# Optimization experiments

Measured on AMD Instinct MI355X. Metric: run time of the kernel, lower is better.

Reference implementation:

```python
import jax, jax.numpy as jnp
import numpy as np

B, L, M = 4, 16384, 256
HID, FDIM, INNER, ODIM = 512, 128, 128, 3
HEADS, DH = 2, 64
NFREQ = 16  # feature_dim // (2 * input_dim)
ALPHA = 10.0
SIGMA_Q = 128.0
SIGMA_LS = (128.0, 32.0, 8.0)


def setup_inputs() -> dict:
    key = jax.random.key(0)
    ks = jax.random.split(key, 16)
    s = 0.02
    nl = len(SIGMA_LS)
    return {
        "x": jax.random.uniform(ks[0], (B, L, 4), jnp.float32),
        "tokens": jax.random.normal(ks[1], (B, M, HID), jnp.float32),
        "w_query": jax.random.normal(ks[2], (FDIM, HID), jnp.float32) * s,
        "b_query": jnp.zeros((HID,), jnp.float32),
        "w_to_q": jax.random.normal(ks[3], (HID, INNER), jnp.float32) * s,
        "w_to_kv": jax.random.normal(ks[4], (HID, 2 * INNER), jnp.float32) * s,
        "w_to_out": jax.random.normal(ks[5], (INNER, HID), jnp.float32) * s,
        "b_to_out": jnp.zeros((HID,), jnp.float32),
        "w_band": jax.random.normal(ks[6], (nl, FDIM, HID), jnp.float32) * s,
        "b_band": jnp.zeros((nl, HID), jnp.float32),
        "w_mod": jax.random.normal(ks[7], (nl, HID, HID), jnp.float32) * s,
        "b_mod": jnp.zeros((nl, HID), jnp.float32),
        "w_hv": jax.random.normal(ks[8], (nl - 1, HID, HID), jnp.float32) * s,
        "b_hv": jnp.zeros((nl - 1, HID), jnp.float32),
        "w_out": jax.random.normal(ks[9], (nl, HID, ODIM), jnp.float32) * s,
        "b_out": jnp.zeros((nl, ODIM), jnp.float32),
        "Dd": 8, "Hh": 16, "Ww": 16, "Tt": 8,
    }


def _calc_gamma(grid, omegas):
    # grid: [L, 4]; omegas: [NFREQ] -> gamma: [L, 4*2*NFREQ] = [L, FDIM]
    arg = jnp.pi * grid[:, :, None] * omegas[None, None, :]
    return jnp.concatenate([jnp.sin(arg), jnp.cos(arg)], axis=-1).reshape(grid.shape[0], -1)


def reference(x, tokens, w_query, b_query, w_to_q, w_to_kv, w_to_out, b_to_out,
              w_band, b_band, w_mod, b_mod, w_hv, b_hv, w_out, b_out, Dd, Hh, Ww, Tt):
    Bn, Ln, _ = x.shape
    m = tokens.shape[1]
    grid = x[0]  # grid shared across batch, exactly as in the torch module (uses x[0])

    # relative-position bias (ALiBi-like) from approximate patch indices
    z_i = (grid[:, 0] * Dd).astype(jnp.int32)
    y_i = (grid[:, 1] * Hh).astype(jnp.int32)
    x_i = (grid[:, 2] * Ww).astype(jnp.int32)
    t_i = (grid[:, 3] * Tt).astype(jnp.int32)
    idx = ((t_i * Dd + z_i) * Hh + y_i) * Ww + x_i  # [L]
    n_tot = Dd * Hh * Ww * Tt
    t = idx.astype(jnp.float32) / n_tot
    tok_pos = (jnp.arange(m, dtype=jnp.float32) + 0.5) / m
    bias = -ALPHA * (t[:, None] - tok_pos[None, :]) ** 2  # [L, m]

    # Fourier-feature query path (shared across batch)
    omegas_q = jnp.logspace(1.0, np.log10(SIGMA_Q), NFREQ, dtype=jnp.float32)
    x_q = jax.nn.relu(_calc_gamma(grid, omegas_q) @ w_query + b_query)  # [L, HID]

    # cross attention with additive bias
    q = (x_q @ w_to_q).reshape(Ln, HEADS, DH).transpose(1, 0, 2)  # [H, L, Dh]
    kv = tokens @ w_to_kv  # [B, m, 2*INNER]
    k, v = jnp.split(kv, 2, axis=-1)
    k = k.reshape(Bn, m, HEADS, DH).transpose(0, 2, 1, 3)  # [B, H, m, Dh]
    v = v.reshape(Bn, m, HEADS, DH).transpose(0, 2, 1, 3)
    sim = jnp.einsum('hld,bhmd->bhlm', q, k) * (DH ** -0.5) + bias[None, None]
    attn = jax.nn.softmax(sim, axis=-1)
    out = jnp.einsum('bhlm,bhmd->bhld', attn, v)
    out = out.transpose(0, 2, 1, 3).reshape(Bn, Ln, HEADS * DH)
    modv = out @ w_to_out + b_to_out  # [B, L, HID]

    # modulated MLP chain with residual hv accumulation
    total = jnp.zeros((Bn, Ln, w_out.shape[-1]), dtype=x.dtype)
    hv = None
    for kk in range(len(SIGMA_LS)):
        omg = jnp.logspace(1.0, np.log10(SIGMA_LS[kk]), NFREQ, dtype=jnp.float32)
        h_l = jax.nn.relu(_calc_gamma(grid, omg) @ w_band[kk] + b_band[kk])  # [L, HID]
        m_l = jax.nn.relu(h_l[None] + modv @ w_mod[kk] + b_mod[kk])  # [B, L, HID]
        if kk == 0:
            hv = m_l
        else:
            hv = jax.nn.relu((m_l + hv) @ w_hv[kk - 1] + b_hv[kk - 1])
        total = total + hv @ w_out[kk] + b_out[kk]
    return total  # [B, L, ODIM]
```

## Files before the change

### kernel.cpp

```cpp
#include <hip/hip_runtime.h>

#define L_N   16384
#define B_N   4
#define M_N   256
#define HID_N 512
#define PI_F  3.14159265358979323846f

typedef short short8 __attribute__((ext_vector_type(8)));
typedef float f32x4 __attribute__((ext_vector_type(4)));

__device__ __forceinline__ ushort f2bf(float f) {
  uint u = __float_as_uint(f);
  uint r = u + 0x7FFF + ((u >> 16) & 1);
  return (ushort)(r >> 16);
}
__device__ __forceinline__ float bf2f(ushort s) {
  return __uint_as_float(((uint)s) << 16);
}
__device__ __forceinline__ void gld_lds16(const void* g, void* s) {
  __builtin_amdgcn_global_load_lds((const __attribute__((address_space(1))) void*)g,
                                   (__attribute__((address_space(3))) void*)s, 16, 0, 0);
}

__global__ __launch_bounds__(256) void k_wt_all(
    const float* __restrict__ w_query, const float* __restrict__ w_to_q,
    const float* __restrict__ w_to_kv, const float* __restrict__ w_to_out,
    const float* __restrict__ w_band, const float* __restrict__ w_mod,
    const float* __restrict__ w_hv,
    ushort* __restrict__ wq_t, ushort* __restrict__ wtq_t,
    ushort* __restrict__ wkv_t, ushort* __restrict__ wto_t,
    ushort* __restrict__ wb_t, ushort* __restrict__ wm_t, ushort* __restrict__ whv_t) {
  __shared__ float t[32][33];
  int tb = blockIdx.x;
  const float* in; ushort* out; int R, C;
  if (tb < 64)        { in = w_query;  out = wq_t;  R = 128; C = 512; }
  else if (tb < 128)  { tb -= 64;  in = w_to_q;   out = wtq_t; R = 512; C = 128; }
  else if (tb < 256)  { tb -= 128; in = w_to_kv;  out = wkv_t; R = 512; C = 256; }
  else if (tb < 320)  { tb -= 256; in = w_to_out; out = wto_t; R = 128; C = 512; }
  else if (tb < 512)  { tb -= 320; int kk = tb >> 6; tb &= 63;
                        in = w_band + (size_t)kk * 65536; out = wb_t + (size_t)kk * 65536; R = 128; C = 512; }
  else if (tb < 1280) { tb -= 512; int kk = tb >> 8; tb &= 255;
                        in = w_mod + (size_t)kk * 262144; out = wm_t + (size_t)kk * 262144; R = 512; C = 512; }
  else                { tb -= 1280; int kk = tb >> 8; tb &= 255;
                        in = w_hv + (size_t)kk * 262144; out = whv_t + (size_t)kk * 262144; R = 512; C = 512; }
  int nbx = C >> 5;
  int bx = (tb % nbx) * 32, by = (tb / nbx) * 32;
  int tx = threadIdx.x & 31, ty = threadIdx.x >> 5;
#pragma unroll
  for (int j = 0; j < 32; j += 8) t[ty + j][tx] = in[(size_t)(by + ty + j) * C + bx + tx];
  __syncthreads();
#pragma unroll
  for (int j = 0; j < 32; j += 8)
    out[(size_t)(bx + ty + j) * R + by + tx] = f2bf(t[tx][ty + j]);
}

__global__ __launch_bounds__(256) void k_cvt(const float* __restrict__ in,
                                             ushort* __restrict__ out, int n4) {
  int i = blockIdx.x * 256 + threadIdx.x;
  if (i >= n4) return;
  float4 v = *(const float4*)&in[(size_t)i * 4];
  ushort* o = &out[(size_t)i * 4];
  o[0] = f2bf(v.x); o[1] = f2bf(v.y); o[2] = f2bf(v.z); o[3] = f2bf(v.w);
}

__global__ __launch_bounds__(256) void k_gamma(const float* __restrict__ x,
                                               ushort* __restrict__ gout) {
  __shared__ float om[16];
  const float lgs[4] = {2.1072099696478683f, 2.1072099696478683f,
                        1.5051499783199058f, 0.9030899869919435f};
  int spec = blockIdx.y;
  float lg = lgs[spec];
  int tid = threadIdx.x;
  if (tid < 16) om[tid] = powf(10.0f, 1.0f + (float)tid * ((lg - 1.0f) * (1.0f / 15.0f)));
  __syncthreads();
  int l0 = blockIdx.x * 16;
  int idx0 = tid * 8;
  int row = idx0 >> 7, f0 = idx0 & 127;
  int c = f0 >> 5;
  float g = x[(size_t)(l0 + row) * 4 + c];
  float base = PI_F * g;
  int w0 = f0 & 31;
  bool is_cos = (w0 >= 16);
  short8 o;
#pragma unroll
  for (int j = 0; j < 8; ++j) {
    int jf = (w0 + j) & 15;
    float arg = base * om[jf];
    float v = is_cos ? __cosf(arg) : __sinf(arg);
    o[j] = (short)f2bf(v);
  }
  *(short8*)&gout[(size_t)spec * L_N * 128 + (size_t)(l0 + row) * 128 + f0] = o;
}

__global__ __launch_bounds__(256) void k_tpos(const float* __restrict__ x,
                                              const int* dD, const int* dH,
                                              const int* dW, const int* dT,
                                              float* __restrict__ tbuf) {
  int l = blockIdx.x * 256 + threadIdx.x;
  float g0 = x[(size_t)l * 4 + 0], g1 = x[(size_t)l * 4 + 1];
  float g2 = x[(size_t)l * 4 + 2], g3 = x[(size_t)l * 4 + 3];
  int Dd = dD[0], Hh = dH[0], Ww = dW[0], Tt = dT[0];
  int zi = (int)(g0 * (float)Dd), yi = (int)(g1 * (float)Hh);
  int xi = (int)(g2 * (float)Ww), ti = (int)(g3 * (float)Tt);
  int idx = ((ti * Dd + zi) * Hh + yi) * Ww + xi;
  tbuf[l] = (float)idx / (float)(Dd * Hh * Ww * Tt);
}

__global__ __launch_bounds__(256, 4) void k_gemm2(
    const ushort* __restrict__ A, long long sA,
    const ushort* __restrict__ Wt, long long sWt,
    const float* __restrict__ bias, int sBias,
    const ushort* __restrict__ add1,
    const ushort* add2, long long sAdd2,
    ushort* C, long long sC,
    const float* __restrict__ wout,
    float* __restrict__ opb,
    int zoff,
    int N, int K, int do_relu,
    int nbx, int nby, int nz) {
  __shared__ __align__(16) ushort S[128 * 64 * 2];
  __shared__ float woutL[384];
  ushort* As = S;
  ushort* Ws = S + 128 * 64;
  int tid = threadIdx.x;
  int lane = tid & 63, wid = tid >> 6;

  int nwg = nbx * nby * nz;
  int gid0 = blockIdx.x;
  int q = nwg >> 3, r = nwg & 7;
  int xcd = gid0 & 7, rank = gid0 >> 3;
  int sid = (xcd < r) ? (xcd * (q + 1) + rank) : (r * (q + 1) + (xcd - r) * q + rank);
  int z = sid / (nbx * nby);
  int rem = sid - z * (nbx * nby);
  int n0 = (rem % nbx) * 128, r0 = (rem / nbx) * 128;

  A += (size_t)z * sA;
  C += (size_t)z * sC;
  const ushort* Wtp = Wt + (size_t)z * sWt;
  const float* biasp = bias ? bias + (size_t)z * sBias : nullptr;
  const ushort* a2p = add2 ? add2 + (size_t)z * sAdd2 : nullptr;
  int wr = wid >> 1, wc = wid & 1;
  int ksm = K >> 6;

  f32x4 acc[4][4];
#pragma unroll
  for (int i = 0; i < 4; ++i)
#pragma unroll
    for (int j = 0; j < 4; ++j) acc[i][j] = (f32x4)0.0f;

  for (int t = 0; t < ksm; ++t) {
#pragma unroll
    for (int j = 0; j < 4; ++j) {
      int sig = j * 256 + wid * 64 + lane;
      int rr = sig >> 3, ph = sig & 7, sl = ph ^ (rr & 7);
      gld_lds16(&A[(size_t)(r0 + rr) * K + t * 64 + sl * 8], &As[(size_t)(j * 256 + wid * 64) * 8]);
      gld_lds16(&Wtp[(size_t)(n0 + rr) * K + t * 64 + sl * 8], &Ws[(size_t)(j * 256 + wid * 64) * 8]);
    }
    __syncthreads();
#pragma unroll
    for (int ks = 0; ks < 2; ++ks) {
      short8 af[4], bg[4];
#pragma unroll
      for (int fm = 0; fm < 4; ++fm) {
        int row = wr * 64 + fm * 16 + (lane & 15);
        af[fm] = *(const short8*)&As[row * 64 + (((ks * 4 + (lane >> 4)) ^ (row & 7)) * 8)];
      }
#pragma unroll
      for (int fn = 0; fn < 4; ++fn) {
        int nl = wc * 64 + fn * 16 + (lane & 15);
        bg[fn] = *(const short8*)&Ws[nl * 64 + (((ks * 4 + (lane >> 4)) ^ (nl & 7)) * 8)];
      }
#pragma unroll
      for (int fm = 0; fm < 4; ++fm)
#pragma unroll
        for (int fn = 0; fn < 4; ++fn)
          acc[fm][fn] = __builtin_amdgcn_mfma_f32_16x16x32_bf16(af[fm], bg[fn], acc[fm][fn], 0, 0, 0);
    }
    __syncthreads();
  }

  if (wout && tid < 128) {
    woutL[tid * 3 + 0] = wout[(size_t)(n0 + tid) * 3 + 0];
    woutL[tid * 3 + 1] = wout[(size_t)(n0 + tid) * 3 + 1];
    woutL[tid * 3 + 2] = wout[(size_t)(n0 + tid) * 3 + 2];
  }

  float* Ls = (float*)S;
  int row = tid >> 3;
  int c0 = (tid & 7) * 16;
#pragma unroll
  for (int fm = 0; fm < 4; ++fm) {
    if (fm) __syncthreads();
#pragma unroll
    for (int fn = 0; fn < 4; ++fn)
#pragma unroll
      for (int reg = 0; reg < 4; ++reg) {
        int lr = wr * 16 + (lane >> 4) * 4 + reg;
        int lc = wc * 64 + fn * 16 + (lane & 15);
        Ls[lr * 132 + lc] = acc[fm][fn][reg];
      }
    __syncthreads();
    int gr = r0 + (row >> 4) * 64 + fm * 16 + (row & 15);
    float so0 = 0.0f, so1 = 0.0f, so2 = 0.0f;
#pragma unroll
    for (int hh = 0; hh < 2; ++hh) {
      int cc = c0 + hh * 8;
      float v[8];
#pragma unroll
      for (int j = 0; j < 8; ++j) v[j] = Ls[row * 132 + cc + j];
      if (biasp) {
#pragma unroll
        for (int j = 0; j < 8; ++j) v[j] += biasp[n0 + cc + j];
      }
      if (add1) {
        short8 a1 = *(const short8*)&add1[(size_t)gr * N + n0 + cc];
#pragma unroll
        for (int j = 0; j < 8; ++j) v[j] += bf2f((ushort)a1[j]);
      }
      if (do_relu) {
#pragma unroll
        for (int j = 0; j < 8; ++j) v[j] = fmaxf(v[j], 0.0f);
      }
      if (a2p) {
        short8 a2 = *(const short8*)&a2p[(size_t)gr * N + n0 + cc];
#pragma unroll
        for (int j = 0; j < 8; ++j) v[j] += bf2f((ushort)a2[j]);
      }
      if (wout) {
#pragma unroll
        for (int j = 0; j < 8; ++j) {
          so0 = fmaf(v[j], woutL[(cc + j) * 3 + 0], so0);
          so1 = fmaf(v[j], woutL[(cc + j) * 3 + 1], so1);
          so2 = fmaf(v[j], woutL[(cc + j) * 3 + 2], so2);
        }
      }
      short8 ov;
#pragma unroll
      for (int j = 0; j < 8; ++j) ov[j] = (short)f2bf(v[j]);
      *(short8*)&C[(size_t)gr * N + n0 + cc] = ov;
    }
    if (wout) {
      so0 += __shfl_down(so0, 4); so1 += __shfl_down(so1, 4); so2 += __shfl_down(so2, 4);
      so0 += __shfl_down(so0, 2); so1 += __shfl_down(so1, 2); so2 += __shfl_down(so2, 2);
      so0 += __shfl_down(so0, 1); so1 += __shfl_down(so1, 1); so2 += __shfl_down(so2, 1);
      if ((tid & 7) == 0) {
        int bx = n0 >> 7;
        size_t oi = (((size_t)bx * 4 + (zoff + z)) * L_N + gr) * 3;
        opb[oi + 0] = so0; opb[oi + 1] = so1; opb[oi + 2] = so2;
      }
    }
  }
}

__global__ __launch_bounds__(256) void k_outred(const float* __restrict__ opb,
                                                const float* __restrict__ b_out,
                                                float* __restrict__ out) {
  int i = blockIdx.x * 256 + threadIdx.x;
  if (i >= B_N * L_N) return;
  float a0 = b_out[0] + b_out[3] + b_out[6];
  float a1 = b_out[1] + b_out[4] + b_out[7];
  float a2 = b_out[2] + b_out[5] + b_out[8];
  const size_t SS = (size_t)4 * B_N * L_N * 3;
#pragma unroll
  for (int slot = 0; slot < 3; ++slot)
#pragma unroll
    for (int bx = 0; bx < 4; ++bx) {
      const float* p = opb + slot * SS + (((size_t)bx * B_N * L_N) + i) * 3;
      a0 += p[0]; a1 += p[1]; a2 += p[2];
    }
  out[(size_t)i * 3 + 0] = a0;
  out[(size_t)i * 3 + 1] = a1;
  out[(size_t)i * 3 + 2] = a2;
}

__global__ __launch_bounds__(256) void k_rearr(const ushort* __restrict__ kvtmp,
                                               ushort* __restrict__ kbuf,
                                               ushort* __restrict__ vtb) {
  int i = blockIdx.x * 256 + threadIdx.x;
  int col = i & 255, row = i >> 8;
  int b = row >> 8, m = row & 255;
  ushort v = kvtmp[i];
  if (col < 128)
    kbuf[((size_t)b * 256 + m) * 128 + col] = v;
  else
    vtb[(size_t)b * 128 * 256 + (size_t)(col - 128) * 256 + m] = v;
}

__global__ __launch_bounds__(256) void k_attn_m(const ushort* __restrict__ qbuf,
                                                const float* __restrict__ tbuf,
                                                const ushort* __restrict__ kbuf,
                                                const ushort* __restrict__ vtb,
                                                ushort* __restrict__ attn) {
  __shared__ __align__(16) ushort Kt[256 * 64];
  __shared__ __align__(16) ushort Vt[64 * 256];
  __shared__ __align__(16) ushort Qs[64 * 64];
  __shared__ __align__(16) ushort Pw[4][16 * 40];
  __shared__ float ts[64];
  int tid = threadIdx.x;
  int lane = tid & 63, wid = tid >> 6;
  int l0 = blockIdx.x * 64;
  int h = blockIdx.y;
  int z = blockIdx.z;
  const ushort* kbuf_b = kbuf + (size_t)z * M_N * 128;
  const ushort* vtb_b = vtb + (size_t)z * 128 * M_N;
  ushort* attn_b = attn + (size_t)z * L_N * 128;
#pragma unroll
  for (int j = 0; j < 8; ++j) {
    int sig = j * 256 + wid * 64 + lane;
    int m = sig >> 3, ph = sig & 7, sl = ph ^ (m & 7);
    gld_lds16(&kbuf_b[(size_t)m * 128 + h * 64 + sl * 8], &Kt[(size_t)(j * 256 + wid * 64) * 8]);
  }
#pragma unroll
  for (int j = 0; j < 8; ++j) {
    int sig = j * 256 + wid * 64 + lane;
    int d = sig >> 5, ph = sig & 31, sl = ph ^ ((d & 7) << 2);
    gld_lds16(&vtb_b[(size_t)(h * 64 + d) * 256 + sl * 8], &Vt[(size_t)(j * 256 + wid * 64) * 8]);
  }
#pragma unroll
  for (int j = 0; j < 2; ++j) {
    int sig = j * 256 + wid * 64 + lane;
    int q = sig >> 3, ph = sig & 7, sl = ph ^ (q & 7);
    gld_lds16(&qbuf[(size_t)(l0 + q) * 128 + h * 64 + sl * 8], &Qs[(size_t)(j * 256 + wid * 64) * 8]);
  }
  if (tid < 64) ts[tid] = tbuf[l0 + tid];
  __syncthreads();

  f32x4 s_acc[16];
#pragma unroll
  for (int fn = 0; fn < 16; ++fn) s_acc[fn] = (f32x4)0.0f;
#pragma unroll
  for (int ks = 0; ks < 2; ++ks) {
    int qrow = wid * 16 + (lane & 15);
    short8 aq = *(const short8*)&Qs[qrow * 64 + (((ks * 4 + (lane >> 4)) ^ (qrow & 7)) * 8)];
#pragma unroll
    for (int fn = 0; fn < 16; ++fn) {
      int m = fn * 16 + (lane & 15);
      short8 bk = *(const short8*)&Kt[m * 64 + (((ks * 4 + (lane >> 4)) ^ (m & 7)) * 8)];
      s_acc[fn] = __builtin_amdgcn_mfma_f32_16x16x32_bf16(aq, bk, s_acc[fn], 0, 0, 0);
    }
  }
  float mx[4] = {-1e30f, -1e30f, -1e30f, -1e30f};
#pragma unroll
  for (int fn = 0; fn < 16; ++fn) {
#pragma unroll
    for (int reg = 0; reg < 4; ++reg) {
      int ql = wid * 16 + (lane >> 4) * 4 + reg;
      int m = fn * 16 + (lane & 15);
      float mp = ((float)m + 0.5f) * (1.0f / 256.0f);
      float d = ts[ql] - mp;
      float v = s_acc[fn][reg] * 0.125f - 10.0f * d * d;
      s_acc[fn][reg] = v;
      mx[reg] = fmaxf(mx[reg], v);
    }
  }
#pragma unroll
  for (int reg = 0; reg < 4; ++reg) {
    mx[reg] = fmaxf(mx[reg], __shfl_xor(mx[reg], 1));
    mx[reg] = fmaxf(mx[reg], __shfl_xor(mx[reg], 2));
    mx[reg] = fmaxf(mx[reg], __shfl_xor(mx[reg], 4));
    mx[reg] = fmaxf(mx[reg], __shfl_xor(mx[reg], 8));
  }
  float sm[4] = {0.0f, 0.0f, 0.0f, 0.0f};
#pragma unroll
  for (int fn = 0; fn < 16; ++fn) {
#pragma unroll
    for (int reg = 0; reg < 4; ++reg) {
      float e = __expf(s_acc[fn][reg] - mx[reg]);
      s_acc[fn][reg] = e;
      sm[reg] += e;
    }
  }
#pragma unroll
  for (int reg = 0; reg < 4; ++reg) {
    sm[reg] += __shfl_xor(sm[reg], 1);
    sm[reg] += __shfl_xor(sm[reg], 2);
    sm[reg] += __shfl_xor(sm[reg], 4);
    sm[reg] += __shfl_xor(sm[reg], 8);
  }
  float inv[4];
#pragma unroll
  for (int reg = 0; reg < 4; ++reg) inv[reg] = 1.0f / sm[reg];

  f32x4 o_acc[4];
#pragma unroll
  for (int fn = 0; fn < 4; ++fn) o_acc[fn] = (f32x4)0.0f;
  for (int kk = 0; kk < 8; ++kk) {
#pragma unroll
    for (int fp = 0; fp < 2; ++fp) {
      int fn = kk * 2 + fp;
#pragma unroll
      for (int reg = 0; reg < 4; ++reg) {
        int ql16 = (lane >> 4) * 4 + reg;
        int mc = fp * 16 + (lane & 15);
        Pw[wid][ql16 * 40 + mc] = f2bf(s_acc[fn][reg] * inv[reg]);
      }
    }
    asm volatile("s_waitcnt lgkmcnt(0)" ::: "memory");
    __builtin_amdgcn_sched_barrier(0);
    short8 pa = *(const short8*)&Pw[wid][(lane & 15) * 40 + (lane >> 4) * 8];
#pragma unroll
    for (int fn = 0; fn < 4; ++fn) {
      int dr = fn * 16 + (lane & 15);
      short8 vb = *(const short8*)&Vt[dr * 256 + (((kk * 4 + (lane >> 4)) ^ ((dr & 7) << 2)) * 8)];
      o_acc[fn] = __builtin_amdgcn_mfma_f32_16x16x32_bf16(pa, vb, o_acc[fn], 0, 0, 0);
    }
    asm volatile("s_waitcnt lgkmcnt(0)" ::: "memory");
    __builtin_amdgcn_sched_barrier(0);
  }
#pragma unroll
  for (int fn = 0; fn < 4; ++fn)
#pragma unroll
    for (int reg = 0; reg < 4; ++reg) {
      int ql = l0 + wid * 16 + (lane >> 4) * 4 + reg;
      attn_b[(size_t)ql * 128 + h * 64 + fn * 16 + (lane & 15)] = f2bf(o_acc[fn][reg]);
    }
}

extern "C" void kernel_launch(void* const* d_in, const int* in_sizes, int n_in,
                              void* d_out, int out_size, void* d_ws, size_t ws_size,
                              hipStream_t stream) {
  const float* x        = (const float*)d_in[0];
  const float* tokens   = (const float*)d_in[1];
  const float* w_query  = (const float*)d_in[2];
  const float* b_query  = (const float*)d_in[3];
  const float* w_to_q   = (const float*)d_in[4];
  const float* w_to_kv  = (const float*)d_in[5];
  const float* w_to_out = (const float*)d_in[6];
  const float* b_to_out = (const float*)d_in[7];
  const float* w_band   = (const float*)d_in[8];
  const float* b_band   = (const float*)d_in[9];
  const float* w_mod    = (const float*)d_in[10];
  const float* b_mod    = (const float*)d_in[11];
  const float* w_hv     = (const float*)d_in[12];
  const float* b_hv     = (const float*)d_in[13];
  const float* w_out    = (const float*)d_in[14];
  const float* b_out    = (const float*)d_in[15];
  const int* Dd = (const int*)d_in[16];
  const int* Hh = (const int*)d_in[17];
  const int* Ww = (const int*)d_in[18];
  const int* Tt = (const int*)d_in[19];
  float* out = (float*)d_out;

  ushort* W = (ushort*)d_ws;
  size_t o = 0;
  auto alloc = [&](size_t n) { ushort* p = W + o; o += n; return p; };
  const size_t big = (size_t)L_N * HID_N;
  const size_t LQ = (size_t)L_N * 128;

  ushort* gamma  = alloc(4 * LQ);
  ushort* qb     = alloc(LQ);
  ushort* attnout= alloc(4 * LQ);
  ushort* tokb   = alloc((size_t)B_N * M_N * HID_N);
  ushort* kbuf   = alloc((size_t)B_N * M_N * 128);
  ushort* vtb    = alloc((size_t)B_N * 128 * M_N);
  ushort* wq_t   = alloc(512 * 128);
  ushort* wtq_t  = alloc(128 * 512);
  ushort* wkv_t  = alloc(256 * 512);
  ushort* wto_t  = alloc(512 * 128);
  ushort* wb_t   = alloc(3 * 512 * 128);
  ushort* wm_t   = alloc(3 * 512 * 512);
  ushort* whv_t  = alloc(2 * 512 * 512);
  float* tbuf    = (float*)alloc(L_N * 2);
  size_t base_u = o;

  int NZ = (ws_size >= (base_u + 9 * big) * sizeof(ushort)) ? 2 : 1;
  ushort* hband = alloc(3 * big);
  ushort* modv  = alloc((size_t)NZ * big);
  ushort* hv    = alloc((size_t)NZ * big);
  ushort* tmp   = alloc((size_t)NZ * big);
  ushort* xq = modv;
  ushort* kvtmp = attnout;
  float* opb = (float*)gamma;

  const long long BG = (long long)big;
  const long long LQs = (long long)LQ;
  const size_t SLOT = (size_t)4 * B_N * L_N * 3;

  k_wt_all<<<dim3(1792), 256, 0, stream>>>(w_query, w_to_q, w_to_kv, w_to_out, w_band, w_mod, w_hv,
                                           wq_t, wtq_t, wkv_t, wto_t, wb_t, wm_t, whv_t);
  k_cvt<<<dim3(512), 256, 0, stream>>>(tokens, tokb, B_N * M_N * HID_N / 4);
  k_gamma<<<dim3(L_N / 16, 4), 256, 0, stream>>>(x, gamma);
  k_tpos<<<dim3(L_N / 256), 256, 0, stream>>>(x, Dd, Hh, Ww, Tt, tbuf);

  k_gemm2<<<dim3(4 * 128), 256, 0, stream>>>(gamma, 0, wq_t, 0, b_query, 0, nullptr, nullptr, 0,
                                             xq, 0, nullptr, nullptr, 0, 512, 128, 1, 4, 128, 1);
  k_gemm2<<<dim3(1 * 128), 256, 0, stream>>>(xq, 0, wtq_t, 0, nullptr, 0, nullptr, nullptr, 0,
                                             qb, 0, nullptr, nullptr, 0, 128, 512, 0, 1, 128, 1);
  k_gemm2<<<dim3(2 * 8), 256, 0, stream>>>(tokb, 0, wkv_t, 0, nullptr, 0, nullptr, nullptr, 0,
                                           kvtmp, 0, nullptr, nullptr, 0, 256, 512, 0, 2, 8, 1);
  k_rearr<<<dim3(1024), 256, 0, stream>>>(kvtmp, kbuf, vtb);
  k_attn_m<<<dim3(L_N / 64, 2, 4), 256, 0, stream>>>(qb, tbuf, kbuf, vtb, attnout);
  k_gemm2<<<dim3(4 * 128 * 3), 256, 0, stream>>>(gamma + LQ, LQs, wb_t, 65536, b_band, 512,
                                                 nullptr, nullptr, 0, hband, BG,
                                                 nullptr, nullptr, 0, 512, 128, 1, 4, 128, 3);

  for (int zoff = 0; zoff < B_N; zoff += NZ) {
    k_gemm2<<<dim3(4 * 128 * NZ), 256, 0, stream>>>(attnout + (size_t)zoff * LQ, LQs, wto_t, 0,
                                                    b_to_out, 0, nullptr, nullptr, 0,
                                                    modv, BG, nullptr, nullptr, 0,
                                                    512, 128, 0, 4, 128, NZ);
    for (int kk = 0; kk < 3; ++kk) {
      if (kk == 0) {
        k_gemm2<<<dim3(4 * 128 * NZ), 256, 0, stream>>>(modv, BG, wm_t, 0, b_mod, 0, hband,
                                                        nullptr, 0, hv, BG,
                                                        w_out, opb, zoff, 512, 512, 1, 4, 128, NZ);
      } else {
        k_gemm2<<<dim3(4 * 128 * NZ), 256, 0, stream>>>(modv, BG, wm_t + (size_t)kk * 262144, 0,
                                                        b_mod + kk * 512, 0, hband + (size_t)kk * big,
                                                        hv, BG, tmp, BG,
                                                        nullptr, nullptr, 0, 512, 512, 1, 4, 128, NZ);
        k_gemm2<<<dim3(4 * 128 * NZ), 256, 0, stream>>>(tmp, BG, whv_t + (size_t)(kk - 1) * 262144, 0,
                                                        b_hv + (kk - 1) * 512, 0, nullptr,
                                                        nullptr, 0, hv, BG,
                                                        w_out + (size_t)kk * 1536, opb + (size_t)kk * SLOT,
                                                        zoff, 512, 512, 1, 4, 128, NZ);
      }
    }
  }
  k_outred<<<dim3((B_N * L_N + 255) / 256), 256, 0, stream>>>(opb, b_out, out);
}
```

Baseline: 448.6 us.

## Fuse first two modulation GEMMs, accumulate output projections in place, batch all samples

Adds a k_mpair kernel that computes the level-0 and level-1 modulation GEMMs together, sharing each A tile across both weight sets. Its epilogue applies both ReLU/hband adds, writes the level-0 output projection, and stores the summed m0+m1 input for the next hv GEMM. The final hv GEMM skips writing its bf16 output, and the per-level output projections now accumulate into one partial buffer, so the reduction kernel reads less data. The workspace is reorganized so all four batches run in one pass when enough space is available, at the cost of read-modify-write on the partial buffer and extra register and LDS pressure in the paired kernel.

```diff
diff --git a/kernel.cpp b/kernel.cpp
--- a/kernel.cpp
+++ b/kernel.cpp
@@ -135,7 +135,7 @@
   int n0 = (rem % nbx) * 128, r0 = (rem / nbx) * 128;
 
   A += (size_t)z * sA;
-  C += (size_t)z * sC;
+  ushort* Cp = C ? C + (size_t)z * sC : nullptr;
   const ushort* Wtp = Wt + (size_t)z * sWt;
   const float* biasp = bias ? bias + (size_t)z * sBias : nullptr;
   const ushort* a2p = add2 ? add2 + (size_t)z * sAdd2 : nullptr;
@@ -234,10 +234,12 @@
           so2 = fmaf(v[j], woutL[(cc + j) * 3 + 2], so2);
         }
       }
-      short8 ov;
-#pragma unroll
-      for (int j = 0; j < 8; ++j) ov[j] = (short)f2bf(v[j]);
-      *(short8*)&C[(size_t)gr * N + n0 + cc] = ov;
+      if (Cp) {
+        short8 ov;
+#pragma unroll
+        for (int j = 0; j < 8; ++j) ov[j] = (short)f2bf(v[j]);
+        *(short8*)&Cp[(size_t)gr * N + n0 + cc] = ov;
+      }
     }
     if (wout) {
       so0 += __shfl_down(so0, 4); so1 += __shfl_down(so1, 4); so2 += __shfl_down(so2, 4);
@@ -246,8 +248,136 @@
       if ((tid & 7) == 0) {
         int bx = n0 >> 7;
         size_t oi = (((size_t)bx * 4 + (zoff + z)) * L_N + gr) * 3;
-        opb[oi + 0] = so0; opb[oi + 1] = so1; opb[oi + 2] = so2;
-      }
+        opb[oi + 0] += so0; opb[oi + 1] += so1; opb[oi + 2] += so2;
+      }
+    }
+  }
+}
+
+__global__ __launch_bounds__(256, 2) void k_mpair(
+    const ushort* __restrict__ modv,
+    const ushort* __restrict__ wm_t,
+    const float* __restrict__ b_mod,
+    const ushort* __restrict__ hband,
+    const float* __restrict__ wout,
+    float* __restrict__ opb, int zoff,
+    ushort* __restrict__ s1,
+    int nbx, int nby, int nz) {
+  __shared__ __align__(16) ushort S[3 * 128 * 64];
+  __shared__ float woutL[384];
+  const size_t big = (size_t)L_N * HID_N;
+  ushort* As = S;
+  ushort* W0 = S + 128 * 64;
+  ushort* W1 = S + 2 * 128 * 64;
+  int tid = threadIdx.x;
+  int lane = tid & 63, wid = tid >> 6;
+
+  int nwg = nbx * nby * nz;
+  int gid0 = blockIdx.x;
+  int q = nwg >> 3, r = nwg & 7;
+  int xcd = gid0 & 7, rank = gid0 >> 3;
+  int sid = (xcd < r) ? (xcd * (q + 1) + rank) : (r * (q + 1) + (xcd - r) * q + rank);
+  int z = sid / (nbx * nby);
+  int rem = sid - z * (nbx * nby);
+  int n0 = (rem % nbx) * 128, r0 = (rem / nbx) * 128;
+
+  const ushort* A = modv + (size_t)z * big;
+  ushort* Cp = s1 + (size_t)z * big;
+  int wr = wid >> 1, wc = wid & 1;
+
+  f32x4 acc0[4][4], acc1[4][4];
+#pragma unroll
+  for (int i = 0; i < 4; ++i)
+#pragma unroll
+    for (int j = 0; j < 4; ++j) { acc0[i][j] = (f32x4)0.0f; acc1[i][j] = (f32x4)0.0f; }
+
+  for (int t = 0; t < 8; ++t) {
+#pragma unroll
+    for (int j = 0; j < 4; ++j) {
+      int sig = j * 256 + wid * 64 + lane;
+      int rr = sig >> 3, ph = sig & 7, sl = ph ^ (rr & 7);
+      gld_lds16(&A[(size_t)(r0 + rr) * 512 + t * 64 + sl * 8], &As[(size_t)sig * 8]);
+      gld_lds16(&wm_t[(size_t)(n0 + rr) * 512 + t * 64 + sl * 8], &W0[(size_t)sig * 8]);
+      gld_lds16(&wm_t[262144 + (size_t)(n0 + rr) * 512 + t * 64 + sl * 8], &W1[(size_t)sig * 8]);
+    }
+    __syncthreads();
+#pragma unroll
+    for (int ks = 0; ks < 2; ++ks) {
+      short8 af[4], bg0[4], bg1[4];
+#pragma unroll
+      for (int fm = 0; fm < 4; ++fm) {
+        int rrow = wr * 64 + fm * 16 + (lane & 15);
+        af[fm] = *(const short8*)&As[rrow * 64 + (((ks * 4 + (lane >> 4)) ^ (rrow & 7)) * 8)];
+      }
+#pragma unroll
+      for (int fn = 0; fn < 4; ++fn) {
+        int nl = wc * 64 + fn * 16 + (lane & 15);
+        int off = nl * 64 + (((ks * 4 + (lane >> 4)) ^ (nl & 7)) * 8);
+        bg0[fn] = *(const short8*)&W0[off];
+        bg1[fn] = *(const short8*)&W1[off];
+      }
+#pragma unroll
+      for (int fm = 0; fm < 4; ++fm)
+#pragma unroll
+        for (int fn = 0; fn < 4; ++fn) {
+          acc0[fm][fn] = __builtin_amdgcn_mfma_f32_16x16x32_bf16(af[fm], bg0[fn], acc0[fm][fn], 0, 0, 0);
+          acc1[fm][fn] = __builtin_amdgcn_mfma_f32_16x16x32_bf16(af[fm], bg1[fn], acc1[fm][fn], 0, 0, 0);
+        }
+    }
+    __syncthreads();
+  }
+
+  if (tid < 128) {
+    woutL[tid * 3 + 0] = wout[(size_t)(n0 + tid) * 3 + 0];
+    woutL[tid * 3 + 1] = wout[(size_t)(n0 + tid) * 3 + 1];
+    woutL[tid * 3 + 2] = wout[(size_t)(n0 + tid) * 3 + 2];
+  }
+
+  float* Ls0 = (float*)S;
+  float* Ls1 = (float*)S + 32 * 132;
+  int row = tid >> 3;
+  int c0 = (tid & 7) * 16;
+#pragma unroll
+  for (int fm = 0; fm < 4; ++fm) {
+    if (fm) __syncthreads();
+#pragma unroll
+    for (int fn = 0; fn < 4; ++fn)
+#pragma unroll
+      for (int reg = 0; reg < 4; ++reg) {
+        int lr = wr * 16 + (lane >> 4) * 4 + reg;
+        int lc = wc * 64 + fn * 16 + (lane & 15);
+        Ls0[lr * 132 + lc] = acc0[fm][fn][reg];
+        Ls1[lr * 132 + lc] = acc1[fm][fn][reg];
+      }
+    __syncthreads();
+    int gr = r0 + (row >> 4) * 64 + fm * 16 + (row & 15);
+    float so0 = 0.0f, so1 = 0.0f, so2 = 0.0f;
+#pragma unroll
+    for (int hh = 0; hh < 2; ++hh) {
+      int cc = c0 + hh * 8;
+      short8 h0 = *(const short8*)&hband[(size_t)gr * 512 + n0 + cc];
+      short8 h1 = *(const short8*)&hband[big + (size_t)gr * 512 + n0 + cc];
+      float v0[8], v1[8];
+#pragma unroll
+      for (int j = 0; j < 8; ++j) {
+        v0[j] = fmaxf(Ls0[row * 132 + cc + j] + b_mod[n0 + cc + j] + bf2f((ushort)h0[j]), 0.0f);
+        v1[j] = fmaxf(Ls1[row * 132 + cc + j] + b_mod[512 + n0 + cc + j] + bf2f((ushort)h1[j]), 0.0f);
+        so0 = fmaf(v0[j], woutL[(cc + j) * 3 + 0], so0);
+        so1 = fmaf(v0[j], woutL[(cc + j) * 3 + 1], so1);
+        so2 = fmaf(v0[j], woutL[(cc + j) * 3 + 2], so2);
+      }
+      short8 ov;
+#pragma unroll
+      for (int j = 0; j < 8; ++j) ov[j] = (short)f2bf(v0[j] + v1[j]);
+      *(short8*)&Cp[(size_t)gr * 512 + n0 + cc] = ov;
+    }
+    so0 += __shfl_down(so0, 4); so1 += __shfl_down(so1, 4); so2 += __shfl_down(so2, 4);
+    so0 += __shfl_down(so0, 2); so1 += __shfl_down(so1, 2); so2 += __shfl_down(so2, 2);
+    so0 += __shfl_down(so0, 1); so1 += __shfl_down(so1, 1); so2 += __shfl_down(so2, 1);
+    if ((tid & 7) == 0) {
+      int bx = n0 >> 7;
+      size_t oi = (((size_t)bx * 4 + (zoff + z)) * L_N + gr) * 3;
+      opb[oi + 0] = so0; opb[oi + 1] = so1; opb[oi + 2] = so2;
     }
   }
 }
@@ -260,14 +390,11 @@
   float a0 = b_out[0] + b_out[3] + b_out[6];
   float a1 = b_out[1] + b_out[4] + b_out[7];
   float a2 = b_out[2] + b_out[5] + b_out[8];
-  const size_t SS = (size_t)4 * B_N * L_N * 3;
-#pragma unroll
-  for (int slot = 0; slot < 3; ++slot)
-#pragma unroll
-    for (int bx = 0; bx < 4; ++bx) {
-      const float* p = opb + slot * SS + (((size_t)bx * B_N * L_N) + i) * 3;
-      a0 += p[0]; a1 += p[1]; a2 += p[2];
-    }
+#pragma unroll
+  for (int bx = 0; bx < 4; ++bx) {
+    const float* p = opb + ((size_t)bx * 4 * L_N + i) * 3;
+    a0 += p[0]; a1 += p[1]; a2 += p[2];
+  }
   out[(size_t)i * 3 + 0] = a0;
   out[(size_t)i * 3 + 1] = a1;
   out[(size_t)i * 3 + 2] = a2;
@@ -319,8 +446,8 @@
 #pragma unroll
   for (int j = 0; j < 2; ++j) {
     int sig = j * 256 + wid * 64 + lane;
-    int q = sig >> 3, ph = sig & 7, sl = ph ^ (q & 7);
-    gld_lds16(&qbuf[(size_t)(l0 + q) * 128 + h * 64 + sl * 8], &Qs[(size_t)(j * 256 + wid * 64) * 8]);
+    int qq = sig >> 3, ph = sig & 7, sl = ph ^ (qq & 7);
+    gld_lds16(&qbuf[(size_t)(l0 + qq) * 128 + h * 64 + sl * 8], &Qs[(size_t)(j * 256 + wid * 64) * 8]);
   }
   if (tid < 64) ts[tid] = tbuf[l0 + tid];
   __syncthreads();
@@ -447,9 +574,7 @@
   const size_t big = (size_t)L_N * HID_N;
   const size_t LQ = (size_t)L_N * 128;
 
-  ushort* gamma  = alloc(4 * LQ);
   ushort* qb     = alloc(LQ);
-  ushort* attnout= alloc(4 * LQ);
   ushort* tokb   = alloc((size_t)B_N * M_N * HID_N);
   ushort* kbuf   = alloc((size_t)B_N * M_N * 128);
   ushort* vtb    = alloc((size_t)B_N * 128 * M_N);
@@ -463,26 +588,41 @@
   float* tbuf    = (float*)alloc(L_N * 2);
   size_t base_u = o;
 
-  int NZ = (ws_size >= (base_u + 9 * big) * sizeof(ushort)) ? 2 : 1;
-  ushort* hband = alloc(3 * big);
-  ushort* modv  = alloc((size_t)NZ * big);
-  ushort* hv    = alloc((size_t)NZ * big);
-  ushort* tmp   = alloc((size_t)NZ * big);
+  int NZ;
+  if (ws_size >= (base_u + 15 * big) * sizeof(ushort)) NZ = 4;
+  else if (ws_size >= (base_u + 10 * big) * sizeof(ushort)) NZ = 2;
+  else NZ = 1;
+
+  ushort *gammaR, *attnout, *s1, *hband, *modv, *hv1;
+  if (NZ == 4) {
+    gammaR  = alloc(4 * big);
+    attnout = alloc(4 * big);
+    hband   = alloc(3 * big);
+    modv    = alloc(4 * big);
+    hv1 = gammaR;
+    s1  = attnout;
+  } else {
+    gammaR  = alloc((size_t)(NZ > 1 ? NZ : 1) * big);
+    attnout = alloc(big);
+    s1      = alloc((size_t)NZ * big);
+    hband   = alloc(3 * big);
+    modv    = alloc((size_t)NZ * big);
+    hv1 = gammaR;
+  }
   ushort* xq = modv;
   ushort* kvtmp = attnout;
-  float* opb = (float*)gamma;
+  float* opb = (float*)qb;
 
   const long long BG = (long long)big;
   const long long LQs = (long long)LQ;
-  const size_t SLOT = (size_t)4 * B_N * L_N * 3;
 
   k_wt_all<<<dim3(1792), 256, 0, stream>>>(w_query, w_to_q, w_to_kv, w_to_out, w_band, w_mod, w_hv,
                                            wq_t, wtq_t, wkv_t, wto_t, wb_t, wm_t, whv_t);
   k_cvt<<<dim3(512), 256, 0, stream>>>(tokens, tokb, B_N * M_N * HID_N / 4);
-  k_gamma<<<dim3(L_N / 16, 4), 256, 0, stream>>>(x, gamma);
+  k_gamma<<<dim3(L_N / 16, 4), 256, 0, stream>>>(x, gammaR);
   k_tpos<<<dim3(L_N / 256), 256, 0, stream>>>(x, Dd, Hh, Ww, Tt, tbuf);
 
-  k_gemm2<<<dim3(4 * 128), 256, 0, stream>>>(gamma, 0, wq_t, 0, b_query, 0, nullptr, nullptr, 0,
+  k_gemm2<<<dim3(4 * 128), 256, 0, stream>>>(gammaR, 0, wq_t, 0, b_query, 0, nullptr, nullptr, 0,
                                              xq, 0, nullptr, nullptr, 0, 512, 128, 1, 4, 128, 1);
   k_gemm2<<<dim3(1 * 128), 256, 0, stream>>>(xq, 0, wtq_t, 0, nullptr, 0, nullptr, nullptr, 0,
                                              qb, 0, nullptr, nullptr, 0, 128, 512, 0, 1, 128, 1);
@@ -490,7 +630,7 @@
                                            kvtmp, 0, nullptr, nullptr, 0, 256, 512, 0, 2, 8, 1);
   k_rearr<<<dim3(1024), 256, 0, stream>>>(kvtmp, kbuf, vtb);
   k_attn_m<<<dim3(L_N / 64, 2, 4), 256, 0, stream>>>(qb, tbuf, kbuf, vtb, attnout);
-  k_gemm2<<<dim3(4 * 128 * 3), 256, 0, stream>>>(gamma + LQ, LQs, wb_t, 65536, b_band, 512,
+  k_gemm2<<<dim3(4 * 128 * 3), 256, 0, stream>>>(gammaR + LQ, LQs, wb_t, 65536, b_band, 512,
                                                  nullptr, nullptr, 0, hband, BG,
                                                  nullptr, nullptr, 0, 512, 128, 1, 4, 128, 3);
 
@@ -499,23 +639,19 @@
                                                     b_to_out, 0, nullptr, nullptr, 0,
                                                     modv, BG, nullptr, nullptr, 0,
                                                     512, 128, 0, 4, 128, NZ);
-    for (int kk = 0; kk < 3; ++kk) {
-      if (kk == 0) {
-        k_gemm2<<<dim3(4 * 128 * NZ), 256, 0, stream>>>(modv, BG, wm_t, 0, b_mod, 0, hband,
-                                                        nullptr, 0, hv, BG,
-                                                        w_out, opb, zoff, 512, 512, 1, 4, 128, NZ);
-      } else {
-        k_gemm2<<<dim3(4 * 128 * NZ), 256, 0, stream>>>(modv, BG, wm_t + (size_t)kk * 262144, 0,
-                                                        b_mod + kk * 512, 0, hband + (size_t)kk * big,
-                                                        hv, BG, tmp, BG,
-                                                        nullptr, nullptr, 0, 512, 512, 1, 4, 128, NZ);
-        k_gemm2<<<dim3(4 * 128 * NZ), 256, 0, stream>>>(tmp, BG, whv_t + (size_t)(kk - 1) * 262144, 0,
-                                                        b_hv + (kk - 1) * 512, 0, nullptr,
-                                                        nullptr, 0, hv, BG,
-                                                        w_out + (size_t)kk * 1536, opb + (size_t)kk * SLOT,
-                                                        zoff, 512, 512, 1, 4, 128, NZ);
-      }
-    }
+    k_mpair<<<dim3(4 * 128 * NZ), 256, 0, stream>>>(modv, wm_t, b_mod, hband, w_out,
+                                                    opb, zoff, s1, 4, 128, NZ);
+    k_gemm2<<<dim3(4 * 128 * NZ), 256, 0, stream>>>(s1, BG, whv_t, 0, b_hv, 0, nullptr, nullptr, 0,
+                                                    hv1, BG, w_out + 1536, opb, zoff,
+                                                    512, 512, 1, 4, 128, NZ);
+    k_gemm2<<<dim3(4 * 128 * NZ), 256, 0, stream>>>(modv, BG, wm_t + 2 * 262144, 0, b_mod + 1024, 0,
+                                                    hband + 2 * big, hv1, BG,
+                                                    s1, BG, nullptr, nullptr, 0,
+                                                    512, 512, 1, 4, 128, NZ);
+    k_gemm2<<<dim3(4 * 128 * NZ), 256, 0, stream>>>(s1, BG, whv_t + 262144, 0, b_hv + 512, 0,
+                                                    nullptr, nullptr, 0, nullptr, 0,
+                                                    w_out + 3072, opb, zoff,
+                                                    512, 512, 1, 4, 128, NZ);
   }
   k_outred<<<dim3((B_N * L_N + 255) / 256), 256, 0, stream>>>(opb, b_out, out);
 }
```

After: 393.6 us (median of 3 runs). -12.2%, faster.
